# Kernel optimization log

Measured on AMD Instinct MI355X. Metric: run time of the kernel, lower is better.

## Reference

```python
import jax, jax.numpy as jnp
import numpy as np

N_HEAD, D_HEAD, EMBED = 16, 64, 1024
B, Q_LEN, MEM_LEN = 2, 1024, 1024
K_LEN = Q_LEN + MEM_LEN  # == r_len
LN_EPS = 1e-3  # keras LayerNormalization default


def rel_shift(x):
    # x: [B, H, q, r]  (Transformer-XL relative shift)
    b, h, q, r = x.shape
    x = jnp.pad(x, ((0, 0), (0, 0), (0, 0), (1, 0)))
    x = x.reshape(b, h, r + 1, q)[:, :, 1:, :]
    return x.reshape(b, h, q, r)


def setup_inputs() -> dict:
    key = jax.random.key(0)
    ks = jax.random.split(key, 12)
    s = 0.02
    w = jax.random.normal(ks[0], (B, Q_LEN, EMBED), jnp.float32)
    r = jax.random.normal(ks[1], (K_LEN, EMBED), jnp.float32)
    member = jax.random.normal(ks[2], (B, MEM_LEN, EMBED), jnp.float32)
    r_w_bias = jax.random.normal(ks[3], (N_HEAD, D_HEAD), jnp.float32) * s
    r_r_bias = jax.random.normal(ks[4], (N_HEAD, D_HEAD), jnp.float32) * s
    # causal mask over [q_len, k_len]: position i may attend to mem + keys <= mem_len+i
    qi = jnp.arange(Q_LEN)[:, None]
    kj = jnp.arange(K_LEN)[None, :]
    attn_mask = (kj > qi + MEM_LEN).astype(jnp.float32)
    Wq = jax.random.normal(ks[5], (EMBED, N_HEAD * D_HEAD), jnp.float32) * s
    Wk = jax.random.normal(ks[6], (EMBED, N_HEAD * D_HEAD), jnp.float32) * s
    Wv = jax.random.normal(ks[7], (EMBED, N_HEAD * D_HEAD), jnp.float32) * s
    Wr = jax.random.normal(ks[8], (EMBED, N_HEAD * D_HEAD), jnp.float32) * s
    Wo = jax.random.normal(ks[9], (N_HEAD * D_HEAD, EMBED), jnp.float32) * s
    ln_gamma = jnp.ones((EMBED,), jnp.float32)
    ln_beta = jnp.zeros((EMBED,), jnp.float32)
    return {"w": w, "r": r, "attn_mask": attn_mask, "r_w_bias": r_w_bias,
            "r_r_bias": r_r_bias, "member": member, "Wq": Wq, "Wk": Wk,
            "Wv": Wv, "Wr": Wr, "Wo": Wo, "ln_gamma": ln_gamma, "ln_beta": ln_beta}


def reference(w, r, attn_mask, r_w_bias, r_r_bias, member, Wq, Wk, Wv, Wr, Wo, ln_gamma, ln_beta):
    b, q_len, _ = w.shape
    cat = jnp.concatenate([member, w], axis=1)          # [B, klen, D]
    klen = cat.shape[1]
    q = (cat @ Wq)[:, -q_len:].reshape(b, q_len, N_HEAD, D_HEAD)
    k = (cat @ Wk).reshape(b, klen, N_HEAD, D_HEAD)
    v = (cat @ Wv).reshape(b, klen, N_HEAD, D_HEAD)
    rr = (r @ Wr).reshape(r.shape[0], N_HEAD, D_HEAD)    # [rlen, H, dh]
    rw_q = q + r_w_bias[None, None]                      # content bias
    rr_q = q + r_r_bias[None, None]                      # position bias
    AC = jnp.einsum('bqhd,bkhd->bhqk', rw_q, k)
    BD = jnp.einsum('bqhd,rhd->bhqr', rr_q, rr)
    BD = rel_shift(BD)
    attn = (AC + BD) / jnp.sqrt(jnp.float32(EMBED))      # note: sqrt(embed), as in source
    m = attn_mask[None, None]                            # [1,1,q,k]
    attn = attn * (1.0 - m) - 1e30 * m
    score = jax.nn.softmax(attn, axis=-1)
    out = jnp.einsum('bhqk,bkhd->bqhd', score, v).reshape(b, q_len, N_HEAD * D_HEAD)
    out = out @ Wo
    x = w + out
    mu = jnp.mean(x, axis=-1, keepdims=True)
    var = jnp.mean(jnp.square(x - mu), axis=-1, keepdims=True)
    return (x - mu) * jax.lax.rsqrt(var + LN_EPS) * ln_gamma + ln_beta
```

## Files before the change

kernel.cpp:

```cpp
#include <hip/hip_runtime.h>


typedef __bf16 bf16;
typedef __bf16 bf16x4 __attribute__((ext_vector_type(4)));
typedef __bf16 bf16x8 __attribute__((ext_vector_type(8)));
typedef float f32x4 __attribute__((ext_vector_type(4)));

#define MFMA16(a, b, c) __builtin_amdgcn_mfma_f32_16x16x32_bf16((a), (b), (c), 0, 0, 0)

constexpr int E = 1024;
constexpr int NH = 16;
constexpr int DH = 64;
constexpr int QL = 1024;
constexpr int ML = 1024;
constexpr int KLEN = 2048;

__device__ __forceinline__ void ldg2lds16(const bf16* g, bf16* l) {
    __builtin_amdgcn_global_load_lds(
        (const __attribute__((address_space(1))) unsigned int*)g,
        (__attribute__((address_space(3))) unsigned int*)l, 16, 0, 0);
}

__device__ __forceinline__ bf16x8 frag8(const bf16* t, int row, int ch) {
    return *(const bf16x8*)(t + row * 64 + ((ch ^ (row & 7)) << 3));
}

__global__ void prep_k(const float* __restrict__ member, const float* __restrict__ w,
                       bf16* __restrict__ cat) {
    int row = blockIdx.x;
    int b = row >> 11, jj = row & 2047;
    const float* src = (jj < ML) ? member + ((size_t)(b * ML + jj)) * E
                                 : w + ((size_t)(b * QL + (jj - ML))) * E;
    float4 f = *(const float4*)(src + threadIdx.x * 4);
    bf16x4 o;
    o[0] = (bf16)f.x; o[1] = (bf16)f.y; o[2] = (bf16)f.z; o[3] = (bf16)f.w;
    *(bf16x4*)(cat + (size_t)row * E + threadIdx.x * 4) = o;
}

__global__ void transpose_k(const float* __restrict__ Wq, const float* __restrict__ Wk,
                            const float* __restrict__ Wv, const float* __restrict__ Wr,
                            const float* __restrict__ Wo, bf16* __restrict__ WqT,
                            bf16* __restrict__ WkT, bf16* __restrict__ WvT,
                            bf16* __restrict__ WrT, bf16* __restrict__ WoT) {
    const float* W; bf16* WT;
    switch (blockIdx.z) {
        case 0: W = Wq; WT = WqT; break;
        case 1: W = Wk; WT = WkT; break;
        case 2: W = Wv; WT = WvT; break;
        case 3: W = Wr; WT = WrT; break;
        default: W = Wo; WT = WoT; break;
    }
    __shared__ float t[32][33];
    int bx = blockIdx.x * 32, by = blockIdx.y * 32;
    int x = threadIdx.x, y = threadIdx.y;
    for (int yy = y; yy < 32; yy += 8)
        t[yy][x] = W[(by + yy) * E + bx + x];
    __syncthreads();
    for (int yy = y; yy < 32; yy += 8)
        WT[(bx + yy) * E + by + x] = (bf16)t[x][yy];
}

__global__ __launch_bounds__(256) void proj_k(
    const bf16* __restrict__ cat, const float* __restrict__ r,
    const bf16* __restrict__ WqT, const bf16* __restrict__ WkT,
    const bf16* __restrict__ WvT, const bf16* __restrict__ WrT,
    const float* __restrict__ rwb, const float* __restrict__ rrb,
    bf16* __restrict__ Qw, bf16* __restrict__ Qr, bf16* __restrict__ Kh,
    bf16* __restrict__ Vt, bf16* __restrict__ RRh) {
    __shared__ __align__(16) bf16 As[128 * 64];
    __shared__ __align__(16) bf16 Bs[128 * 64];
    const int tid = threadIdx.x;
    const int wave = tid >> 6, lane = tid & 63, quad = lane >> 4, l16 = lane & 15;

    int id = blockIdx.x, zone, base;
    if (id < 128) { zone = 0; base = 0; }
    else if (id < 384) { zone = 1; base = 128; }
    else if (id < 640) { zone = 2; base = 384; }
    else { zone = 3; base = 640; }
    const int lid = id - base;
    const int bn = (lid & 7) * 128, bm = (lid >> 3) * 128;
    const bf16* Bt = (zone == 0) ? WqT : (zone == 1) ? WkT : (zone == 2) ? WvT : WrT;
    const int wm = (wave >> 1) * 64, wn = (wave & 1) * 64;

    f32x4 acc[4][4] = {};

    for (int kk = 0; kk < E; kk += 64) {
        if (zone == 3) {
            int srw = tid >> 3, cch = tid & 7;
            for (int c = 0; c < 4; ++c) {
                int row = c * 32 + srw;
                const float* ap = r + (size_t)(bm + row) * E + kk + cch * 8;
                float4 f0 = *(const float4*)ap;
                float4 f1 = *(const float4*)(ap + 4);
                bf16x8 v;
                v[0] = (bf16)f0.x; v[1] = (bf16)f0.y; v[2] = (bf16)f0.z; v[3] = (bf16)f0.w;
                v[4] = (bf16)f1.x; v[5] = (bf16)f1.y; v[6] = (bf16)f1.z; v[7] = (bf16)f1.w;
                *(bf16x8*)(As + row * 64 + ((cch ^ (row & 7)) << 3)) = v;
            }
        } else {
            for (int issue = 0; issue < 4; ++issue) {
                int q = (issue * 4 + wave) * 64 + lane;
                int row = q >> 3, cs = (q & 7) ^ ((q >> 3) & 7);
                int gm = bm + row;
                const bf16* ap;
                if (zone == 0) {
                    int b = gm >> 10;
                    ap = cat + ((size_t)(b * 2048 + 1024 + (gm & 1023))) * E;
                } else {
                    ap = cat + (size_t)gm * E;
                }
                ldg2lds16(ap + kk + cs * 8, As + (issue * 4 + wave) * 512);
            }
        }
        for (int issue = 0; issue < 4; ++issue) {
            int q = (issue * 4 + wave) * 64 + lane;
            int row = q >> 3, cs = (q & 7) ^ ((q >> 3) & 7);
            ldg2lds16(Bt + (size_t)(bn + row) * E + kk + cs * 8,
                      Bs + (issue * 4 + wave) * 512);
        }
        __syncthreads();
        for (int ks = 0; ks < 64; ks += 32) {
            bf16x8 af[4], bfr[4];
            for (int mt = 0; mt < 4; ++mt)
                af[mt] = frag8(As, wm + mt * 16 + l16, (ks >> 3) + quad);
            for (int nt = 0; nt < 4; ++nt)
                bfr[nt] = frag8(Bs, wn + nt * 16 + l16, (ks >> 3) + quad);
            for (int mt = 0; mt < 4; ++mt)
                for (int nt = 0; nt < 4; ++nt)
                    acc[mt][nt] = MFMA16(af[mt], bfr[nt], acc[mt][nt]);
        }
        __syncthreads();
    }

    if (zone == 2) {
        bf16* buf = ((wave < 2) ? As : Bs) + (wave & 1) * 4096;
        for (int mt = 0; mt < 4; ++mt)
            for (int nt = 0; nt < 4; ++nt)
                for (int rr = 0; rr < 4; ++rr) {
                    int lr = mt * 16 + quad * 4 + rr;
                    int lc = nt * 16 + l16;
                    buf[lr * 64 + (((lc >> 3) ^ (lr & 7)) << 3) + (lc & 7)] =
                        (bf16)acc[mt][nt][rr];
                }
        int h = (bn + wn) >> 6;
        int gmw = bm + wm;
        int b = gmw >> 11, jb = gmw & 2047;
        for (int dp = 0; dp < 8; ++dp) {
            int dl = dp * 8 + (lane >> 3);
            int jl = (lane & 7) * 8;
            bf16x8 tmp;
            for (int jj = 0; jj < 8; ++jj) {
                int rw = jl + jj;
                tmp[jj] = buf[rw * 64 + (((dl >> 3) ^ (rw & 7)) << 3) + (dl & 7)];
            }
            *(bf16x8*)(Vt + (((size_t)(b * NH + h) * DH + dl) * KLEN) + jb + jl) = tmp;
        }
        return;
    }

    for (int mt = 0; mt < 4; ++mt)
        for (int nt = 0; nt < 4; ++nt)
            for (int rr = 0; rr < 4; ++rr) {
                int row = bm + wm + mt * 16 + quad * 4 + rr;
                int col = bn + wn + nt * 16 + l16;
                float v = acc[mt][nt][rr];
                if (zone == 0) {
                    int b = row >> 10, i = row & 1023;
                    int h = col >> 6, d = col & 63;
                    size_t o = (((size_t)(b * NH + h) * QL) + i) * DH + d;
                    Qw[o] = (bf16)((v + rwb[col]) * 0.03125f);
                    Qr[o] = (bf16)((v + rrb[col]) * 0.03125f);
                } else if (zone == 1) {
                    int b = row >> 11, j = row & 2047;
                    int h = col >> 6, d = col & 63;
                    Kh[(((size_t)(b * NH + h) * KLEN) + j) * DH + d] = (bf16)v;
                } else {
                    int h = col >> 6, d = col & 63;
                    RRh[(((size_t)h * KLEN) + row) * DH + d] = (bf16)v;
                }
            }
}

__global__ __launch_bounds__(256) void attn_k(
    const bf16* __restrict__ Qw, const bf16* __restrict__ Qr,
    const bf16* __restrict__ Kh, const bf16* __restrict__ Vt,
    const bf16* __restrict__ RRh, bf16* __restrict__ AttO) {
    __shared__ __align__(16) bf16 Ks[2][64 * 64];
    __shared__ __align__(16) bf16 Vs[2][64 * 64];
    __shared__ __align__(16) bf16 RRing[3][64 * 64];
    __shared__ __align__(16) bf16 UB[4][16 * 88];

    const int tid = threadIdx.x;
    const int wave = tid >> 6, lane = tid & 63, quad = lane >> 4, l16 = lane & 15;
    const int id = blockIdx.x;
    const int b = id >> 8, h = (id >> 4) & 15;
    const int qt = (id < 256) ? (id & 15) : (15 - (id & 15));
    const int i0 = qt * 64;

    const bf16* Qwb = Qw + ((size_t)(b * NH + h) * QL) * DH;
    const bf16* Qrb = Qr + ((size_t)(b * NH + h) * QL) * DH;
    const bf16* Kb = Kh + ((size_t)(b * NH + h) * KLEN) * DH;
    const bf16* Vb = Vt + ((size_t)(b * NH + h) * DH) * KLEN;
    const bf16* Rb = RRh + ((size_t)h * KLEN) * DH;

    bf16x8 qw0, qw1, qr0, qr1;
    {
        int i = i0 + wave * 16 + l16;
        qw0 = *(const bf16x8*)(Qwb + (size_t)i * DH + quad * 8);
        qw1 = *(const bf16x8*)(Qwb + (size_t)i * DH + 32 + quad * 8);
        qr0 = *(const bf16x8*)(Qrb + (size_t)i * DH + quad * 8);
        qr1 = *(const bf16x8*)(Qrb + (size_t)i * DH + 32 + quad * 8);
    }

    float lpart[4] = {0.f, 0.f, 0.f, 0.f};
    f32x4 oacc[4] = {};

    const int ntiles = qt + 17;
    const int cbase = 15 - qt;
    const int ptbase = 3 - wave;

    auto stage_kv = [&](int t) {
        const int j0 = t * 64;
        bf16* Kd = Ks[t & 1];
        bf16* Vd = Vs[t & 1];
        for (int issue = 0; issue < 2; ++issue) {
            int q = (issue * 4 + wave) * 64 + lane;
            int row = q >> 3, cs = (q & 7) ^ ((q >> 3) & 7);
            ldg2lds16(Kb + (size_t)(j0 + row) * DH + cs * 8,
                      Kd + (issue * 4 + wave) * 512);
            ldg2lds16(Vb + (size_t)row * KLEN + j0 + cs * 8,
                      Vd + (issue * 4 + wave) * 512);
        }
    };
    auto stage_rr = [&](int c) {
        bf16* Rd = RRing[c % 3];
        for (int issue = 0; issue < 2; ++issue) {
            int q = (issue * 4 + wave) * 64 + lane;
            int row = q >> 3, cs = (q & 7) ^ ((q >> 3) & 7);
            int pr = c * 64 + row;
            pr = pr > KLEN - 1 ? KLEN - 1 : pr;
            ldg2lds16(Rb + (size_t)pr * DH + cs * 8, Rd + (issue * 4 + wave) * 512);
        }
    };

    stage_kv(0);
    stage_rr(cbase);
    stage_rr(cbase + 1);
    __syncthreads();

    for (int t = 0; t < ntiles; ++t) {
        const bf16* Kt = Ks[t & 1];
        const bf16* Vl = Vs[t & 1];
        const bf16* Rlo = RRing[(cbase + t) % 3];
        const bf16* Rhi = RRing[(cbase + t + 1) % 3];
        if (t + 1 < ntiles) {
            stage_kv(t + 1);
            stage_rr(cbase + t + 2);
        }

        for (int pi = 0; pi < 5; ++pi) {
            int pt = ptbase + pi;
            const bf16* Rsrc = (pt < 4) ? Rlo : Rhi;
            int rrow = (pt & 3) * 16 + l16;
            f32x4 bacc = {};
            bacc = MFMA16(qr0, frag8(Rsrc, rrow, quad), bacc);
            bacc = MFMA16(qr1, frag8(Rsrc, rrow, 4 + quad), bacc);
            for (int rr = 0; rr < 4; ++rr)
                UB[wave][(quad * 4 + rr) * 88 + pi * 16 + l16] = (bf16)bacc[rr];
        }

        f32x4 sacc[4];
        for (int nt = 0; nt < 4; ++nt) {
            f32x4 a = {};
            a = MFMA16(qw0, frag8(Kt, nt * 16 + l16, quad), a);
            a = MFMA16(qw1, frag8(Kt, nt * 16 + l16, 4 + quad), a);
            sacc[nt] = a;
        }

        float sv[4][4];
        const bool lastt = (t == ntiles - 1);
        for (int nt = 0; nt < 4; ++nt)
            for (int rr = 0; rr < 4; ++rr) {
                int lr = quad * 4 + rr;
                int col = nt * 16 + l16 + 15 - lr;
                float bdv = (float)UB[wave][lr * 88 + col];
                float p = __expf(sacc[nt][rr] + bdv);
                if (lastt) {
                    int i = i0 + wave * 16 + lr;
                    int j = t * 64 + nt * 16 + l16;
                    if (j > i + ML) p = 0.f;
                }
                sv[nt][rr] = p;
                lpart[rr] += p;
            }

        for (int nt = 0; nt < 4; ++nt)
            for (int rr = 0; rr < 4; ++rr)
                UB[wave][(quad * 4 + rr) * 88 + nt * 16 + l16] = (bf16)sv[nt][rr];

        for (int c = 0; c < 2; ++c) {
            bf16x8 pa = *(const bf16x8*)(&UB[wave][l16 * 88 + c * 32 + quad * 8]);
            for (int nt = 0; nt < 4; ++nt) {
                bf16x8 vb = frag8(Vl, nt * 16 + l16, c * 4 + quad);
                oacc[nt] = MFMA16(pa, vb, oacc[nt]);
            }
        }
        __syncthreads();
    }

    float linv[4];
    for (int rr = 0; rr < 4; ++rr) {
        float v = lpart[rr];
        v += __shfl_xor(v, 1);
        v += __shfl_xor(v, 2);
        v += __shfl_xor(v, 4);
        v += __shfl_xor(v, 8);
        linv[rr] = 1.f / v;
    }

    for (int nt = 0; nt < 4; ++nt)
        for (int rr = 0; rr < 4; ++rr) {
            int i = i0 + wave * 16 + quad * 4 + rr;
            int d = nt * 16 + l16;
            float ov = oacc[nt][rr] * linv[rr];
            AttO[((size_t)(b * QL + i)) * E + h * DH + d] = (bf16)ov;
        }
}

__global__ __launch_bounds__(256) void gemm_o(
    const bf16* __restrict__ A, const bf16* __restrict__ Bt,
    const float* __restrict__ resid, float* __restrict__ Xout) {
    __shared__ __align__(16) bf16 As[128 * 64];
    __shared__ __align__(16) bf16 Bs[128 * 64];
    const int tid = threadIdx.x;
    const int wave = tid >> 6, lane = tid & 63, quad = lane >> 4, l16 = lane & 15;
    const int bm = blockIdx.y * 128, bn = blockIdx.x * 128;
    const int wm = (wave >> 1) * 64, wn = (wave & 1) * 64;

    f32x4 acc[4][4] = {};

    for (int kk = 0; kk < E; kk += 64) {
        for (int issue = 0; issue < 4; ++issue) {
            int q = (issue * 4 + wave) * 64 + lane;
            int row = q >> 3, cs = (q & 7) ^ ((q >> 3) & 7);
            ldg2lds16(A + (size_t)(bm + row) * E + kk + cs * 8,
                      As + (issue * 4 + wave) * 512);
            ldg2lds16(Bt + (size_t)(bn + row) * E + kk + cs * 8,
                      Bs + (issue * 4 + wave) * 512);
        }
        __syncthreads();
        for (int ks = 0; ks < 64; ks += 32) {
            bf16x8 af[4], bfr[4];
            for (int mt = 0; mt < 4; ++mt)
                af[mt] = frag8(As, wm + mt * 16 + l16, (ks >> 3) + quad);
            for (int nt = 0; nt < 4; ++nt)
                bfr[nt] = frag8(Bs, wn + nt * 16 + l16, (ks >> 3) + quad);
            for (int mt = 0; mt < 4; ++mt)
                for (int nt = 0; nt < 4; ++nt)
                    acc[mt][nt] = MFMA16(af[mt], bfr[nt], acc[mt][nt]);
        }
        __syncthreads();
    }

    for (int mt = 0; mt < 4; ++mt)
        for (int nt = 0; nt < 4; ++nt)
            for (int rr = 0; rr < 4; ++rr) {
                int row = bm + wm + mt * 16 + quad * 4 + rr;
                int col = bn + wn + nt * 16 + l16;
                Xout[(size_t)row * E + col] =
                    acc[mt][nt][rr] + resid[(size_t)row * E + col];
            }
}

__global__ __launch_bounds__(256) void ln_k(const float* __restrict__ X,
                                            const float* __restrict__ gamma,
                                            const float* __restrict__ beta,
                                            float* __restrict__ out) {
    const int row = blockIdx.x;
    const int tid = threadIdx.x;
    const float* xr = X + (size_t)row * E;
    float xv[4], s = 0.f, q = 0.f;
    for (int c = 0; c < 4; ++c) {
        float v = xr[c * 256 + tid];
        xv[c] = v;
        s += v;
        q += v * v;
    }
    for (int off = 32; off > 0; off >>= 1) {
        s += __shfl_down(s, off);
        q += __shfl_down(q, off);
    }
    __shared__ float rs[4], rq[4];
    int wave = tid >> 6, lane = tid & 63;
    if (lane == 0) { rs[wave] = s; rq[wave] = q; }
    __syncthreads();
    float S = rs[0] + rs[1] + rs[2] + rs[3];
    float Q = rq[0] + rq[1] + rq[2] + rq[3];
    float mean = S * (1.f / E);
    float var = fmaxf(Q * (1.f / E) - mean * mean, 0.f);
    float rstd = rsqrtf(var + 1e-3f);
    for (int c = 0; c < 4; ++c) {
        int col = c * 256 + tid;
        out[(size_t)row * E + col] =
            (xv[c] - mean) * rstd * gamma[col] + beta[col];
    }
}

extern "C" void kernel_launch(void* const* d_in, const int* in_sizes, int n_in,
                              void* d_out, int out_size, void* d_ws,
                              size_t ws_size, hipStream_t stream) {
    (void)in_sizes; (void)n_in; (void)out_size; (void)ws_size;
    const float* w = (const float*)d_in[0];
    const float* r = (const float*)d_in[1];
    const float* rwb = (const float*)d_in[3];
    const float* rrb = (const float*)d_in[4];
    const float* member = (const float*)d_in[5];
    const float* Wq = (const float*)d_in[6];
    const float* Wk = (const float*)d_in[7];
    const float* Wv = (const float*)d_in[8];
    const float* Wr = (const float*)d_in[9];
    const float* Wo = (const float*)d_in[10];
    const float* gamma = (const float*)d_in[11];
    const float* beta = (const float*)d_in[12];
    float* out = (float*)d_out;

    char* ws = (char*)d_ws;
    const size_t MB = 1024 * 1024;
    bf16* WqT = (bf16*)(ws + 0 * MB);
    bf16* WkT = (bf16*)(ws + 2 * MB);
    bf16* WvT = (bf16*)(ws + 4 * MB);
    bf16* WrT = (bf16*)(ws + 6 * MB);
    bf16* WoT = (bf16*)(ws + 8 * MB);
    bf16* cat = (bf16*)(ws + 10 * MB);
    bf16* AttO = (bf16*)(ws + 14 * MB);
    bf16* Qw = (bf16*)(ws + 18 * MB);
    bf16* Qr = (bf16*)(ws + 22 * MB);
    float* X = (float*)(ws + 18 * MB);
    bf16* Kh = (bf16*)(ws + 26 * MB);
    bf16* Vt = (bf16*)(ws + 34 * MB);
    bf16* RRh = (bf16*)(ws + 42 * MB);

    prep_k<<<4096, 256, 0, stream>>>(member, w, cat);
    transpose_k<<<dim3(32, 32, 5), dim3(32, 8), 0, stream>>>(
        Wq, Wk, Wv, Wr, Wo, WqT, WkT, WvT, WrT, WoT);

    proj_k<<<768, 256, 0, stream>>>(cat, r, WqT, WkT, WvT, WrT, rwb, rrb, Qw,
                                    Qr, Kh, Vt, RRh);

    attn_k<<<512, 256, 0, stream>>>(Qw, Qr, Kh, Vt, RRh, AttO);

    gemm_o<<<dim3(8, 16), 256, 0, stream>>>(AttO, WoT, w, X);
    ln_k<<<2048, 256, 0, stream>>>(X, gamma, beta, out);
}
```

Before: 267.9 us.

## Split attention and output GEMM along K, double-buffer projection GEMM loads

The attention kernel now launches two blocks per (batch, head, query-tile) task. Each block handles half of the key tiles and writes an unnormalized partial output and a partial row sum. A new combine kernel adds the two halves and normalizes them into AttO. The output projection GEMM is split into two K halves written to separate fp32 buffers; the LayerNorm kernel sums both partials plus the residual. Both proj_k and gemm_o now double-buffer their LDS tiles so the next tile's loads overlap the current MFMA work. The aim is better CU occupancy and balance for the uneven causal attention work and the small output GEMM. The cost is extra partial-buffer traffic, one more kernel launch, and doubled LDS use.

```diff
diff --git a/kernel.cpp b/kernel.cpp
--- a/kernel.cpp
+++ b/kernel.cpp
@@ -67,8 +67,8 @@
     const float* __restrict__ rwb, const float* __restrict__ rrb,
     bf16* __restrict__ Qw, bf16* __restrict__ Qr, bf16* __restrict__ Kh,
     bf16* __restrict__ Vt, bf16* __restrict__ RRh) {
-    __shared__ __align__(16) bf16 As[128 * 64];
-    __shared__ __align__(16) bf16 Bs[128 * 64];
+    __shared__ __align__(16) bf16 As[2][128 * 64];
+    __shared__ __align__(16) bf16 Bs[2][128 * 64];
     const int tid = threadIdx.x;
     const int wave = tid >> 6, lane = tid & 63, quad = lane >> 4, l16 = lane & 15;
 
@@ -84,7 +84,10 @@
 
     f32x4 acc[4][4] = {};
 
-    for (int kk = 0; kk < E; kk += 64) {
+    auto stage = [&](int s) {
+        const int kk = s * 64;
+        bf16* Ad = As[s & 1];
+        bf16* Bd = Bs[s & 1];
         if (zone == 3) {
             int srw = tid >> 3, cch = tid & 7;
             for (int c = 0; c < 4; ++c) {
@@ -95,7 +98,7 @@
                 bf16x8 v;
                 v[0] = (bf16)f0.x; v[1] = (bf16)f0.y; v[2] = (bf16)f0.z; v[3] = (bf16)f0.w;
                 v[4] = (bf16)f1.x; v[5] = (bf16)f1.y; v[6] = (bf16)f1.z; v[7] = (bf16)f1.w;
-                *(bf16x8*)(As + row * 64 + ((cch ^ (row & 7)) << 3)) = v;
+                *(bf16x8*)(Ad + row * 64 + ((cch ^ (row & 7)) << 3)) = v;
             }
         } else {
             for (int issue = 0; issue < 4; ++issue) {
@@ -109,22 +112,29 @@
                 } else {
                     ap = cat + (size_t)gm * E;
                 }
-                ldg2lds16(ap + kk + cs * 8, As + (issue * 4 + wave) * 512);
+                ldg2lds16(ap + kk + cs * 8, Ad + (issue * 4 + wave) * 512);
             }
         }
         for (int issue = 0; issue < 4; ++issue) {
             int q = (issue * 4 + wave) * 64 + lane;
             int row = q >> 3, cs = (q & 7) ^ ((q >> 3) & 7);
             ldg2lds16(Bt + (size_t)(bn + row) * E + kk + cs * 8,
-                      Bs + (issue * 4 + wave) * 512);
-        }
-        __syncthreads();
+                      Bd + (issue * 4 + wave) * 512);
+        }
+    };
+
+    stage(0);
+    __syncthreads();
+    for (int s = 0; s < 16; ++s) {
+        if (s + 1 < 16) stage(s + 1);
+        const bf16* Ac = As[s & 1];
+        const bf16* Bc = Bs[s & 1];
         for (int ks = 0; ks < 64; ks += 32) {
             bf16x8 af[4], bfr[4];
             for (int mt = 0; mt < 4; ++mt)
-                af[mt] = frag8(As, wm + mt * 16 + l16, (ks >> 3) + quad);
+                af[mt] = frag8(Ac, wm + mt * 16 + l16, (ks >> 3) + quad);
             for (int nt = 0; nt < 4; ++nt)
-                bfr[nt] = frag8(Bs, wn + nt * 16 + l16, (ks >> 3) + quad);
+                bfr[nt] = frag8(Bc, wn + nt * 16 + l16, (ks >> 3) + quad);
             for (int mt = 0; mt < 4; ++mt)
                 for (int nt = 0; nt < 4; ++nt)
                     acc[mt][nt] = MFMA16(af[mt], bfr[nt], acc[mt][nt]);
@@ -133,7 +143,7 @@
     }
 
     if (zone == 2) {
-        bf16* buf = ((wave < 2) ? As : Bs) + (wave & 1) * 4096;
+        bf16* buf = &As[0][0] + wave * 4096;
         for (int mt = 0; mt < 4; ++mt)
             for (int nt = 0; nt < 4; ++nt)
                 for (int rr = 0; rr < 4; ++rr) {
@@ -184,7 +194,8 @@
 __global__ __launch_bounds__(256) void attn_k(
     const bf16* __restrict__ Qw, const bf16* __restrict__ Qr,
     const bf16* __restrict__ Kh, const bf16* __restrict__ Vt,
-    const bf16* __restrict__ RRh, bf16* __restrict__ AttO) {
+    const bf16* __restrict__ RRh, bf16* __restrict__ Opart,
+    float* __restrict__ Lpart) {
     __shared__ __align__(16) bf16 Ks[2][64 * 64];
     __shared__ __align__(16) bf16 Vs[2][64 * 64];
     __shared__ __align__(16) bf16 RRing[3][64 * 64];
@@ -193,9 +204,13 @@
     const int tid = threadIdx.x;
     const int wave = tid >> 6, lane = tid & 63, quad = lane >> 4, l16 = lane & 15;
     const int id = blockIdx.x;
-    const int b = id >> 8, h = (id >> 4) & 15;
-    const int qt = (id < 256) ? (id & 15) : (15 - (id & 15));
+    const int task = id >> 1, half = id & 1;
+    const int b = task >> 8, h = (task >> 4) & 15, qt = task & 15;
     const int i0 = qt * 64;
+    const int T = qt + 17;
+    const int h0 = (T + 1) >> 1;
+    const int t0 = half ? h0 : 0;
+    const int tEnd = half ? T : h0;
 
     const bf16* Qwb = Qw + ((size_t)(b * NH + h) * QL) * DH;
     const bf16* Qrb = Qr + ((size_t)(b * NH + h) * QL) * DH;
@@ -215,7 +230,6 @@
     float lpart[4] = {0.f, 0.f, 0.f, 0.f};
     f32x4 oacc[4] = {};
 
-    const int ntiles = qt + 17;
     const int cbase = 15 - qt;
     const int ptbase = 3 - wave;
 
@@ -243,17 +257,17 @@
         }
     };
 
-    stage_kv(0);
-    stage_rr(cbase);
-    stage_rr(cbase + 1);
+    stage_kv(t0);
+    stage_rr(cbase + t0);
+    stage_rr(cbase + t0 + 1);
     __syncthreads();
 
-    for (int t = 0; t < ntiles; ++t) {
+    for (int t = t0; t < tEnd; ++t) {
         const bf16* Kt = Ks[t & 1];
         const bf16* Vl = Vs[t & 1];
         const bf16* Rlo = RRing[(cbase + t) % 3];
         const bf16* Rhi = RRing[(cbase + t + 1) % 3];
-        if (t + 1 < ntiles) {
+        if (t + 1 < tEnd) {
             stage_kv(t + 1);
             stage_rr(cbase + t + 2);
         }
@@ -278,7 +292,7 @@
         }
 
         float sv[4][4];
-        const bool lastt = (t == ntiles - 1);
+        const bool lastt = (t == T - 1);
         for (int nt = 0; nt < 4; ++nt)
             for (int rr = 0; rr < 4; ++rr) {
                 int lr = quad * 4 + rr;
@@ -308,53 +322,82 @@
         __syncthreads();
     }
 
-    float linv[4];
     for (int rr = 0; rr < 4; ++rr) {
         float v = lpart[rr];
         v += __shfl_xor(v, 1);
         v += __shfl_xor(v, 2);
         v += __shfl_xor(v, 4);
         v += __shfl_xor(v, 8);
-        linv[rr] = 1.f / v;
-    }
-
-    for (int nt = 0; nt < 4; ++nt)
-        for (int rr = 0; rr < 4; ++rr) {
-            int i = i0 + wave * 16 + quad * 4 + rr;
-            int d = nt * 16 + l16;
-            float ov = oacc[nt][rr] * linv[rr];
-            AttO[((size_t)(b * QL + i)) * E + h * DH + d] = (bf16)ov;
-        }
+        if (l16 == 0) Lpart[(size_t)id * 64 + wave * 16 + quad * 4 + rr] = v;
+        for (int nt = 0; nt < 4; ++nt)
+            Opart[(size_t)id * 4096 + (wave * 16 + quad * 4 + rr) * 64 + nt * 16 +
+                  l16] = (bf16)oacc[nt][rr];
+    }
+}
+
+__global__ __launch_bounds__(256) void combine_k(const bf16* __restrict__ Opart,
+                                                 const float* __restrict__ Lpart,
+                                                 bf16* __restrict__ AttO) {
+    const int task = blockIdx.x;
+    const int b = task >> 8, h = (task >> 4) & 15, qt = task & 15;
+    const int i0 = qt * 64;
+    const int t = threadIdx.x;
+    const int row = t >> 2, d0 = (t & 3) * 16;
+    size_t g0 = (size_t)task * 2, g1 = g0 + 1;
+    float linv = 1.f / (Lpart[g0 * 64 + row] + Lpart[g1 * 64 + row]);
+    bf16x8 a0 = *(const bf16x8*)(Opart + g0 * 4096 + row * 64 + d0);
+    bf16x8 a1 = *(const bf16x8*)(Opart + g0 * 4096 + row * 64 + d0 + 8);
+    bf16x8 b0 = *(const bf16x8*)(Opart + g1 * 4096 + row * 64 + d0);
+    bf16x8 b1 = *(const bf16x8*)(Opart + g1 * 4096 + row * 64 + d0 + 8);
+    bf16x8 o0, o1;
+    for (int k = 0; k < 8; ++k) {
+        o0[k] = (bf16)(((float)a0[k] + (float)b0[k]) * linv);
+        o1[k] = (bf16)(((float)a1[k] + (float)b1[k]) * linv);
+    }
+    bf16* dst = AttO + ((size_t)(b * QL + i0 + row)) * E + h * DH + d0;
+    *(bf16x8*)dst = o0;
+    *(bf16x8*)(dst + 8) = o1;
 }
 
 __global__ __launch_bounds__(256) void gemm_o(
     const bf16* __restrict__ A, const bf16* __restrict__ Bt,
-    const float* __restrict__ resid, float* __restrict__ Xout) {
-    __shared__ __align__(16) bf16 As[128 * 64];
-    __shared__ __align__(16) bf16 Bs[128 * 64];
+    float* __restrict__ Xp) {
+    __shared__ __align__(16) bf16 As[2][128 * 64];
+    __shared__ __align__(16) bf16 Bs[2][128 * 64];
     const int tid = threadIdx.x;
     const int wave = tid >> 6, lane = tid & 63, quad = lane >> 4, l16 = lane & 15;
     const int bm = blockIdx.y * 128, bn = blockIdx.x * 128;
+    const int kbase = blockIdx.z * 512;
     const int wm = (wave >> 1) * 64, wn = (wave & 1) * 64;
 
     f32x4 acc[4][4] = {};
 
-    for (int kk = 0; kk < E; kk += 64) {
+    auto stage = [&](int s) {
+        const int kk = kbase + s * 64;
+        bf16* Ad = As[s & 1];
+        bf16* Bd = Bs[s & 1];
         for (int issue = 0; issue < 4; ++issue) {
             int q = (issue * 4 + wave) * 64 + lane;
             int row = q >> 3, cs = (q & 7) ^ ((q >> 3) & 7);
             ldg2lds16(A + (size_t)(bm + row) * E + kk + cs * 8,
-                      As + (issue * 4 + wave) * 512);
+                      Ad + (issue * 4 + wave) * 512);
             ldg2lds16(Bt + (size_t)(bn + row) * E + kk + cs * 8,
-                      Bs + (issue * 4 + wave) * 512);
-        }
-        __syncthreads();
+                      Bd + (issue * 4 + wave) * 512);
+        }
+    };
+
+    stage(0);
+    __syncthreads();
+    for (int s = 0; s < 8; ++s) {
+        if (s + 1 < 8) stage(s + 1);
+        const bf16* Ac = As[s & 1];
+        const bf16* Bc = Bs[s & 1];
         for (int ks = 0; ks < 64; ks += 32) {
             bf16x8 af[4], bfr[4];
             for (int mt = 0; mt < 4; ++mt)
-                af[mt] = frag8(As, wm + mt * 16 + l16, (ks >> 3) + quad);
+                af[mt] = frag8(Ac, wm + mt * 16 + l16, (ks >> 3) + quad);
             for (int nt = 0; nt < 4; ++nt)
-                bfr[nt] = frag8(Bs, wn + nt * 16 + l16, (ks >> 3) + quad);
+                bfr[nt] = frag8(Bc, wn + nt * 16 + l16, (ks >> 3) + quad);
             for (int mt = 0; mt < 4; ++mt)
                 for (int nt = 0; nt < 4; ++nt)
                     acc[mt][nt] = MFMA16(af[mt], bfr[nt], acc[mt][nt]);
@@ -362,26 +405,30 @@
         __syncthreads();
     }
 
+    float* Xz = Xp + (size_t)blockIdx.z * 2048 * 1024;
     for (int mt = 0; mt < 4; ++mt)
         for (int nt = 0; nt < 4; ++nt)
             for (int rr = 0; rr < 4; ++rr) {
                 int row = bm + wm + mt * 16 + quad * 4 + rr;
                 int col = bn + wn + nt * 16 + l16;
-                Xout[(size_t)row * E + col] =
-                    acc[mt][nt][rr] + resid[(size_t)row * E + col];
-            }
-}
-
-__global__ __launch_bounds__(256) void ln_k(const float* __restrict__ X,
+                Xz[(size_t)row * E + col] = acc[mt][nt][rr];
+            }
+}
+
+__global__ __launch_bounds__(256) void ln_k(const float* __restrict__ Xp,
+                                            const float* __restrict__ resid,
                                             const float* __restrict__ gamma,
                                             const float* __restrict__ beta,
                                             float* __restrict__ out) {
     const int row = blockIdx.x;
     const int tid = threadIdx.x;
-    const float* xr = X + (size_t)row * E;
+    const float* x0 = Xp + (size_t)row * E;
+    const float* x1 = Xp + (size_t)2048 * 1024 + (size_t)row * E;
+    const float* xr = resid + (size_t)row * E;
     float xv[4], s = 0.f, q = 0.f;
     for (int c = 0; c < 4; ++c) {
-        float v = xr[c * 256 + tid];
+        int col = c * 256 + tid;
+        float v = x0[col] + x1[col] + xr[col];
         xv[c] = v;
         s += v;
         q += v * v;
@@ -432,10 +479,12 @@
     bf16* WrT = (bf16*)(ws + 6 * MB);
     bf16* WoT = (bf16*)(ws + 8 * MB);
     bf16* cat = (bf16*)(ws + 10 * MB);
+    bf16* Opart = (bf16*)(ws + 0 * MB);
+    float* Lpart = (float*)(ws + 10 * MB);
     bf16* AttO = (bf16*)(ws + 14 * MB);
     bf16* Qw = (bf16*)(ws + 18 * MB);
     bf16* Qr = (bf16*)(ws + 22 * MB);
-    float* X = (float*)(ws + 18 * MB);
+    float* Xp = (float*)(ws + 18 * MB);
     bf16* Kh = (bf16*)(ws + 26 * MB);
     bf16* Vt = (bf16*)(ws + 34 * MB);
     bf16* RRh = (bf16*)(ws + 42 * MB);
@@ -447,8 +496,9 @@
     proj_k<<<768, 256, 0, stream>>>(cat, r, WqT, WkT, WvT, WrT, rwb, rrb, Qw,
                                     Qr, Kh, Vt, RRh);
 
-    attn_k<<<512, 256, 0, stream>>>(Qw, Qr, Kh, Vt, RRh, AttO);
-
-    gemm_o<<<dim3(8, 16), 256, 0, stream>>>(AttO, WoT, w, X);
-    ln_k<<<2048, 256, 0, stream>>>(X, gamma, beta, out);
-}
+    attn_k<<<1024, 256, 0, stream>>>(Qw, Qr, Kh, Vt, RRh, Opart, Lpart);
+    combine_k<<<512, 256, 0, stream>>>(Opart, Lpart, AttO);
+
+    gemm_o<<<dim3(8, 16, 2), 256, 0, stream>>>(AttO, WoT, Xp);
+    ln_k<<<2048, 256, 0, stream>>>(Xp, w, gamma, beta, out);
+}
```

New measurement: 529.6 us. 1.98x slower.
